# Performance work log

Hardware: AMD Instinct MI355X
Metric: run time of the kernel (lower is better)

The kernel has to match this reference:

```python
import jax, jax.numpy as jnp
import numpy as np

B, U, L, H, M = 4, 16, 128, 768, 256   # docs, utterances/doc, tokens/utt, hidden, mentions/doc
HID = 150                               # Score MLP hidden dim
N_CLUSTERS = 32


def setup_inputs() -> dict:
    key = jax.random.key(0)
    ks = jax.random.split(key, 8)
    hidden = jax.random.normal(ks[0], (B, U, L, H), jnp.float32)

    rng = np.random.default_rng(0)
    span_utt = rng.integers(0, U, (B, M))
    span_start = rng.integers(0, L - 8, (B, M))
    span_end = span_start + rng.integers(1, 9, (B, M))  # span length in [1, 8]

    # coreference labels: label[i, j] = 1 iff j is a true antecedent (j < i, same cluster);
    # if mention i has no antecedent, label[i, i] = 1 (the epsilon / new-entity slot).
    clusters = rng.integers(0, N_CLUSTERS, (B, M))
    same = clusters[:, :, None] == clusters[:, None, :]
    ant = same & np.tril(np.ones((M, M), bool), -1)
    labels = ant.astype(np.float32)
    diag = np.arange(M)
    labels[:, diag, diag] = (~ant.any(-1)).astype(np.float32)

    scale = 0.02
    W1 = jax.random.normal(ks[1], (3 * H, HID), jnp.float32) * scale
    W2 = jax.random.normal(ks[2], (HID, HID), jnp.float32) * scale
    W3 = jax.random.normal(ks[3], (HID, 1), jnp.float32) * scale
    return {
        "hidden": hidden,
        "span_utt": jnp.asarray(span_utt, jnp.int32),
        "span_start": jnp.asarray(span_start, jnp.int32),
        "span_end": jnp.asarray(span_end, jnp.int32),
        "labels": jnp.asarray(labels),
        "W1": W1, "b1": jnp.zeros((HID,), jnp.float32),
        "W2": W2, "b2": jnp.zeros((HID,), jnp.float32),
        "W3": W3, "b3": jnp.zeros((1,), jnp.float32),
    }


def reference(hidden, span_utt, span_start, span_end, labels, W1, b1, W2, b2, W3, b3):
    # ---- span mean-pooling (EntityEncoder, aggr='mean') ----
    pos = jnp.arange(L)
    mask = (pos[None, None, :] >= span_start[..., None]) & (pos[None, None, :] < span_end[..., None])
    w = mask.astype(hidden.dtype) / (span_end - span_start)[..., None].astype(hidden.dtype)  # [B,M,L]
    gathered = jnp.take_along_axis(hidden, span_utt[:, :, None, None], axis=1)  # [B,M,L,H]
    pooled = jnp.einsum('bml,bmlh->bmh', w, gathered)  # [B,M,H]

    # ---- pairwise antecedent scoring (PairScorer / Score MLP, dropout=eval) ----
    ii, jj = np.tril_indices(M, -1)  # static pair indices, P = M(M-1)/2
    # concat(i_g, j_g, i_g*j_g) @ W1  ==  i_g@W1a + j_g@W1b + (i_g*j_g)@W1c
    W1a, W1b, W1c = W1[:H], W1[H:2 * H], W1[2 * H:]
    hi = pooled @ W1a   # [B,M,HID]
    hj = pooled @ W1b   # [B,M,HID]
    prod = pooled[:, ii] * pooled[:, jj]                    # [B,P,H]
    h1 = jax.nn.relu(hi[:, ii] + hj[:, jj] + prod @ W1c + b1)
    h2 = jax.nn.relu(h1 @ W2 + b2)
    s = (h2 @ W3 + b3)[..., 0]  # [B,P]

    # ---- per-mention ragged softmax, padded to [M, M] with -1000 ----
    # row i has logits s_ij for j<i plus epsilon=0 at j=i (diagonal of zeros matrix)
    logits = jnp.zeros((B, M, M), hidden.dtype).at[:, ii, jj].set(s)
    valid = jnp.tril(jnp.ones((M, M), bool))
    probs = jax.nn.softmax(jnp.where(valid, logits, -1e30), axis=-1)
    probs = jnp.where(valid, probs, jnp.asarray(-1000.0, hidden.dtype))

    # ---- compute_loss ----
    eps = 1e-8
    prob_sum = jnp.sum(jnp.clip(probs * labels, eps, 1.0 - eps), axis=-1)  # [B,M]
    loss = -jnp.sum(jnp.log(prob_sum))
    return loss
```

## Files before the change

kernel.cpp:

```cpp
#include <hip/hip_runtime.h>
#include <hip/hip_bf16.h>

#define B_ 4
#define U_ 16
#define L_ 128
#define H_ 768
#define M_ 256
#define HID_ 150

typedef _Float16 half8 __attribute__((ext_vector_type(8)));
typedef _Float16 half4t __attribute__((ext_vector_type(4)));
typedef float floatx4 __attribute__((ext_vector_type(4)));
typedef float floatx16 __attribute__((ext_vector_type(16)));

__global__ __launch_bounds__(256) void prep_kernel(
    const float* __restrict__ W1, const float* __restrict__ W2,
    const float* __restrict__ b2, const float* __restrict__ W3,
    _Float16* __restrict__ W1cs, _Float16* __restrict__ W2s,
    _Float16* __restrict__ W1abs, float2* __restrict__ bw)
{
    int idx = blockIdx.x * 256 + threadIdx.x;
    if (blockIdx.x == 0 && threadIdx.x < 160) {
        int n = threadIdx.x;
        bw[n] = (n < HID_) ? make_float2(b2[n], W3[n]) : make_float2(0.f, 0.f);
    }
    if (idx < 122880) {
        int k = idx / 160, n = idx - k * 160;
        float v = (n < HID_) ? W1[(size_t)(2 * H_ + k) * HID_ + n] : 0.f;
        W1cs[(k >> 4) * 2560 + (n >> 5) * 512 +
             (((n & 31) | (((k >> 3) & 1) << 5)) << 3) + (k & 7)] = (_Float16)v;
        return;
    }
    idx -= 122880;
    if (idx < 25600) {
        int k = idx / 160, n = idx - k * 160;
        float v = (k < HID_ && n < HID_) ? W2[(size_t)k * HID_ + n] : 0.f;
        W2s[(k >> 4) * 2560 + (n >> 5) * 512 +
            (((n & 31) | (((k >> 3) & 1) << 5)) << 3) + (k & 7)] = (_Float16)v;
        return;
    }
    idx -= 25600;
    if (idx < 245760) {
        int k = idx / 320, n = idx - k * 320;
        float v = 0.f;
        if (n < HID_) v = W1[(size_t)k * HID_ + n];
        else if (n >= 160 && n < 160 + HID_) v = W1[(size_t)(H_ + k) * HID_ + (n - 160)];
        W1abs[(k >> 5) * 10240 + (n >> 4) * 512 +
              (((n & 15) | (((k >> 3) & 3) << 4)) << 3) + (k & 7)] = (_Float16)v;
    }
}

__global__ __launch_bounds__(256) void pool_kernel(
    const float* __restrict__ hidden, const int* __restrict__ sutt,
    const int* __restrict__ sstart, const int* __restrict__ send,
    _Float16* __restrict__ pooledh)
{
    const int bm = blockIdx.x * 4 + (threadIdx.x >> 6);
    const int lane = threadIdx.x & 63;
    const int b  = bm >> 8;
    const int u  = sutt[bm];
    const int st = sstart[bm];
    const int en = send[bm];
    const float inv = 1.0f / (float)(en - st);
    const float* src = hidden + ((size_t)(b * U_ + u) * L_) * H_ + lane * 12;
    float4 s[3];
    #pragma unroll
    for (int q = 0; q < 3; ++q) s[q] = make_float4(0.f, 0.f, 0.f, 0.f);
    for (int l = st; l < en; ++l) {
        const float* p = src + (size_t)l * H_;
        #pragma unroll
        for (int q = 0; q < 3; ++q) {
            float4 v = *(const float4*)(p + q * 4);
            s[q].x += v.x; s[q].y += v.y; s[q].z += v.z; s[q].w += v.w;
        }
    }
    _Float16* gp = pooledh + (size_t)bm * H_ + lane * 12;
    #pragma unroll
    for (int q = 0; q < 3; ++q) {
        half4t hv;
        hv[0] = (_Float16)(s[q].x * inv); hv[1] = (_Float16)(s[q].y * inv);
        hv[2] = (_Float16)(s[q].z * inv); hv[3] = (_Float16)(s[q].w * inv);
        *(half4t*)(gp + q * 4) = hv;
    }
}

__global__ __launch_bounds__(256) void hihj_kernel(
    const _Float16* __restrict__ pooledh, const float* __restrict__ b1,
    const _Float16* __restrict__ W1abs,
    float* __restrict__ hiF, float* __restrict__ hjT)
{
    __shared__ __align__(16) _Float16 spool[16 * 776];
    const int blk = blockIdx.x;
    const int tid = threadIdx.x;
    for (int e = tid; e < 16 * 96; e += 256) {
        int r = e / 96, c = e - r * 96;
        *(half8*)&spool[r * 776 + c * 8] =
            *(const half8*)&pooledh[(size_t)(blk * 16 + r) * H_ + c * 8];
    }
    __syncthreads();

    const int w = tid >> 6, lane = tid & 63;
    const int g = lane >> 4, l15 = lane & 15;
    floatx4 acc[5];
    #pragma unroll
    for (int u5 = 0; u5 < 5; ++u5) acc[u5] = (floatx4){0.f, 0.f, 0.f, 0.f};
    const _Float16* aB = &spool[l15 * 776 + g * 8];
    for (int kc = 0; kc < 24; ++kc) {
        half8 av = *(const half8*)(aB + kc * 32);
        #pragma unroll
        for (int u5 = 0; u5 < 5; ++u5) {
            const int u = w * 5 + u5;
            half8 bv = *(const half8*)(W1abs + (size_t)((kc * 20 + u) * 64 + lane) * 8);
            acc[u5] = __builtin_amdgcn_mfma_f32_16x16x32_f16(av, bv, acc[u5], 0, 0, 0);
        }
    }
    const int row0 = blk * 16 + g * 4;
    #pragma unroll
    for (int u5 = 0; u5 < 5; ++u5) {
        const int n = (w * 5 + u5) * 16 + l15;
        if (n < HID_) {
            float b1v = b1[n];
            #pragma unroll
            for (int r = 0; r < 4; ++r)
                hiF[(size_t)(row0 + r) * 160 + n] = acc[u5][r] + b1v;
        } else if (n >= 160 && n < 160 + HID_) {
            *(float4*)&hjT[(size_t)(n - 160) * 1024 + row0] =
                make_float4(acc[u5][0], acc[u5][1], acc[u5][2], acc[u5][3]);
        }
    }
}

__global__ __launch_bounds__(64, 1) void pair_mlp_kernel(
    const _Float16* __restrict__ pooledh,
    const float* __restrict__ hiF, const float* __restrict__ hjT,
    const _Float16* __restrict__ W1cs, const _Float16* __restrict__ W2s,
    const float2* __restrict__ bw, const float* __restrict__ b3,
    float* __restrict__ logits)
{
    __shared__ __align__(16) _Float16 h1L[2 * 32 * 170];

    int q = blockIdx.x;
    const int b = q / 576;
    int r = q - b * 576;
    int jt = 0;
    while (r >= 128 - 16 * jt) { r -= 128 - 16 * jt; ++jt; }
    const int p = 16 * jt + r;
    const int i0 = 2 * p, j0 = jt * 32;
    const int bm = b * M_;
    const int lane = threadIdx.x & 63;
    const int c31 = lane & 31;
    const int hw = lane >> 5;

    const _Float16* pjp  = pooledh + (size_t)(bm + j0 + c31) * H_ + (hw << 3);
    const _Float16* pip0 = pooledh + (size_t)(bm + i0) * H_ + (hw << 3);
    const _Float16* pip1 = pooledh + (size_t)(bm + i0 + 1) * H_ + (hw << 3);

    floatx16 acc1[2][5];
    #pragma unroll
    for (int t = 0; t < 2; ++t)
        #pragma unroll
        for (int t1 = 0; t1 < 5; ++t1)
            #pragma unroll
            for (int e = 0; e < 16; ++e) acc1[t][t1][e] = 0.f;

    half8 Apj0[2], Apj1[2], Ai00[2], Ai01[2], Ai10[2], Ai11[2];
    half8 Wf[2][10];
    #pragma unroll
    for (int c = 0; c < 2; ++c) {
        const int kb = c * 32;
        Apj0[c] = *(const half8*)(pjp + kb);
        Apj1[c] = *(const half8*)(pjp + kb + 16);
        Ai00[c] = *(const half8*)(pip0 + kb);
        Ai01[c] = *(const half8*)(pip0 + kb + 16);
        Ai10[c] = *(const half8*)(pip1 + kb);
        Ai11[c] = *(const half8*)(pip1 + kb + 16);
        const _Float16* wb = W1cs + (size_t)c * 5120 + lane * 8;
        #pragma unroll
        for (int u = 0; u < 10; ++u) Wf[c][u] = *(const half8*)(wb + u * 512);
    }

    for (int kc = 0; kc < 24; ++kc) {
        const int cur = kc & 1;
        half8 npj0, npj1, ni00, ni01, ni10, ni11, nW[10];
        if (kc < 22) {
            const int kb = (kc + 2) * 32;
            npj0 = *(const half8*)(pjp + kb);
            npj1 = *(const half8*)(pjp + kb + 16);
            ni00 = *(const half8*)(pip0 + kb);
            ni01 = *(const half8*)(pip0 + kb + 16);
            ni10 = *(const half8*)(pip1 + kb);
            ni11 = *(const half8*)(pip1 + kb + 16);
            const _Float16* wb = W1cs + (size_t)(kc + 2) * 5120 + lane * 8;
            #pragma unroll
            for (int u = 0; u < 10; ++u) nW[u] = *(const half8*)(wb + u * 512);
        }
        #pragma unroll
        for (int h = 0; h < 2; ++h) {
            half8 pj = h ? Apj1[cur] : Apj0[cur];
            half8 a0 = (h ? Ai01[cur] : Ai00[cur]) * pj;
            half8 a1 = (h ? Ai11[cur] : Ai10[cur]) * pj;
            #pragma unroll
            for (int t1 = 0; t1 < 5; ++t1) {
                half8 wf = Wf[cur][h * 5 + t1];
                acc1[0][t1] = __builtin_amdgcn_mfma_f32_32x32x16_f16(
                    wf, a0, acc1[0][t1], 0, 0, 0);
                acc1[1][t1] = __builtin_amdgcn_mfma_f32_32x32x16_f16(
                    wf, a1, acc1[1][t1], 0, 0, 0);
            }
        }
        if (kc < 22) {
            Apj0[cur] = npj0; Apj1[cur] = npj1;
            Ai00[cur] = ni00; Ai01[cur] = ni01;
            Ai10[cur] = ni10; Ai11[cur] = ni11;
            #pragma unroll
            for (int u = 0; u < 10; ++u) Wf[cur][u] = nW[u];
        }
    }

    #pragma unroll
    for (int t1 = 0; t1 < 5; ++t1) {
        #pragma unroll
        for (int qd = 0; qd < 4; ++qd) {
            const int n1 = t1 * 32 + 8 * qd + 4 * hw;
            float hj0 = hjT[(size_t)(n1 + 0) * 1024 + bm + j0 + c31];
            float hj1 = hjT[(size_t)(n1 + 1) * 1024 + bm + j0 + c31];
            float hj2 = hjT[(size_t)(n1 + 2) * 1024 + bm + j0 + c31];
            float hj3 = hjT[(size_t)(n1 + 3) * 1024 + bm + j0 + c31];
            #pragma unroll
            for (int t = 0; t < 2; ++t) {
                float4 hiv = *(const float4*)&hiF[(size_t)(bm + i0 + t) * 160 + n1];
                half4t hv;
                hv[0] = (_Float16)fmaxf(acc1[t][t1][4 * qd + 0] + hiv.x + hj0, 0.f);
                hv[1] = (_Float16)fmaxf(acc1[t][t1][4 * qd + 1] + hiv.y + hj1, 0.f);
                hv[2] = (_Float16)fmaxf(acc1[t][t1][4 * qd + 2] + hiv.z + hj2, 0.f);
                hv[3] = (_Float16)fmaxf(acc1[t][t1][4 * qd + 3] + hiv.w + hj3, 0.f);
                *(half4t*)&h1L[(t * 32 + c31) * 170 + n1] = hv;
            }
        }
    }
    __syncthreads();

    const float b3v = b3[0];
    #pragma unroll
    for (int t = 0; t < 2; ++t) {
        floatx16 acc2[5];
        #pragma unroll
        for (int t2 = 0; t2 < 5; ++t2)
            #pragma unroll
            for (int e = 0; e < 16; ++e) acc2[t2][e] = 0.f;

        half8 W2b[2][5], h1b[2];
        #pragma unroll
        for (int c = 0; c < 2; ++c) {
            const _Float16* wb = W2s + (size_t)(c * 5) * 512 + lane * 8;
            #pragma unroll
            for (int t2 = 0; t2 < 5; ++t2) W2b[c][t2] = *(const half8*)(wb + t2 * 512);
            h1b[c] = *(const half8*)&h1L[(t * 32 + c31) * 170 + c * 16 + hw * 8];
        }
        for (int kc2 = 0; kc2 < 10; ++kc2) {
            const int cur = kc2 & 1;
            half8 nw[5], nh;
            if (kc2 < 8) {
                const _Float16* wb = W2s + (size_t)((kc2 + 2) * 5) * 512 + lane * 8;
                #pragma unroll
                for (int t2 = 0; t2 < 5; ++t2) nw[t2] = *(const half8*)(wb + t2 * 512);
                nh = *(const half8*)&h1L[(t * 32 + c31) * 170 + (kc2 + 2) * 16 + hw * 8];
            }
            #pragma unroll
            for (int t2 = 0; t2 < 5; ++t2)
                acc2[t2] = __builtin_amdgcn_mfma_f32_32x32x16_f16(
                    W2b[cur][t2], h1b[cur], acc2[t2], 0, 0, 0);
            if (kc2 < 8) {
                #pragma unroll
                for (int t2 = 0; t2 < 5; ++t2) W2b[cur][t2] = nw[t2];
                h1b[cur] = nh;
            }
        }

        float sown = 0.f;
        #pragma unroll
        for (int t2 = 0; t2 < 5; ++t2) {
            #pragma unroll
            for (int qd = 0; qd < 4; ++qd) {
                const int n2 = t2 * 32 + 8 * qd + 4 * hw;
                float4 bw01 = *(const float4*)&bw[n2];
                float4 bw23 = *(const float4*)&bw[n2 + 2];
                sown += fmaxf(acc2[t2][4 * qd + 0] + bw01.x, 0.f) * bw01.y;
                sown += fmaxf(acc2[t2][4 * qd + 1] + bw01.z, 0.f) * bw01.w;
                sown += fmaxf(acc2[t2][4 * qd + 2] + bw23.x, 0.f) * bw23.y;
                sown += fmaxf(acc2[t2][4 * qd + 3] + bw23.z, 0.f) * bw23.w;
            }
        }
        float s = sown + __shfl_xor(sown, 32);
        const int i = i0 + t;
        const int j = j0 + c31;
        if (lane < 32 && j < i)
            logits[(size_t)(bm + i) * M_ + j] = s + b3v;
    }
}

__global__ __launch_bounds__(256) void loss_kernel(
    const float* __restrict__ logits, const float* __restrict__ labels,
    float* __restrict__ out)
{
    const int bm = blockIdx.x;
    const int i  = bm & (M_ - 1);
    const int j  = threadIdx.x;
    __shared__ float red[4];
    __shared__ float bcast;

    float val = (j < i) ? logits[(size_t)bm * M_ + j]
                        : ((j == i) ? 0.0f : -1e30f);

    float m = val;
    #pragma unroll
    for (int off = 32; off >= 1; off >>= 1) m = fmaxf(m, __shfl_down(m, off, 64));
    const int wave = j >> 6, lane = j & 63;
    if (lane == 0) red[wave] = m;
    __syncthreads();
    if (j == 0) bcast = fmaxf(fmaxf(red[0], red[1]), fmaxf(red[2], red[3]));
    __syncthreads();
    const float mm = bcast;

    float e = (j <= i) ? expf(val - mm) : 0.0f;
    float s = e;
    #pragma unroll
    for (int off = 32; off >= 1; off >>= 1) s += __shfl_down(s, off, 64);
    __syncthreads();
    if (lane == 0) red[wave] = s;
    __syncthreads();
    if (j == 0) bcast = red[0] + red[1] + red[2] + red[3];
    __syncthreads();
    const float ssum = bcast;

    float prob = (j <= i) ? (e / ssum) : -1000.0f;
    float lab = labels[(size_t)bm * M_ + j];
    float tv = prob * lab;
    tv = fminf(fmaxf(tv, 1e-8f), 1.0f - 1e-8f);
    float rs = tv;
    #pragma unroll
    for (int off = 32; off >= 1; off >>= 1) rs += __shfl_down(rs, off, 64);
    __syncthreads();
    if (lane == 0) red[wave] = rs;
    __syncthreads();
    if (j == 0) atomicAdd(out, -logf(red[0] + red[1] + red[2] + red[3]));
}

extern "C" void kernel_launch(void* const* d_in, const int* in_sizes, int n_in,
                              void* d_out, int out_size, void* d_ws, size_t ws_size,
                              hipStream_t stream)
{
    const float* hidden = (const float*)d_in[0];
    const int*   sutt   = (const int*)d_in[1];
    const int*   sstart = (const int*)d_in[2];
    const int*   send   = (const int*)d_in[3];
    const float* labels = (const float*)d_in[4];
    const float* W1     = (const float*)d_in[5];
    const float* b1     = (const float*)d_in[6];
    const float* W2     = (const float*)d_in[7];
    const float* b2     = (const float*)d_in[8];
    const float* W3     = (const float*)d_in[9];
    const float* b3     = (const float*)d_in[10];

    float* ws = (float*)d_ws;
    float*    hiF     = ws;
    float*    hjT     = ws + 163840;
    float*    logits  = ws + 327680;
    float2*   bw      = (float2*)(ws + 589824);
    _Float16* pooledh = (_Float16*)(ws + 590144);
    _Float16* W1cs    = (_Float16*)(ws + 983360);
    _Float16* W2s     = (_Float16*)(ws + 1106240);
    _Float16* W1abs   = (_Float16*)(ws + 1119040);
    float* out = (float*)d_out;

    hipMemsetAsync(d_out, 0, sizeof(float), stream);

    prep_kernel<<<dim3(1540), 256, 0, stream>>>(W1, W2, b2, W3,
                                                W1cs, W2s, W1abs, bw);
    pool_kernel<<<dim3(256), 256, 0, stream>>>(hidden, sutt, sstart, send, pooledh);
    hihj_kernel<<<dim3(64), 256, 0, stream>>>(pooledh, b1, W1abs, hiF, hjT);
    pair_mlp_kernel<<<dim3(576 * B_), 64, 0, stream>>>(pooledh, hiF, hjT,
                                                       W1cs, W2s, bw, b3, logits);
    loss_kernel<<<dim3(B_ * M_), 256, 0, stream>>>(logits, labels, out);
}
```

Baseline: 213.7 us.

## Split pair MLP across two waves sharing W1c tiles staged in LDS

The pair MLP block grows from one wave to two, each handling one of the two i-rows. The W1c weight tiles are no longer loaded into every wave's registers. They are now double-buffered in LDS through global_load_lds, so both waves share one copy of each tile. This cuts per-wave register pressure so two blocks can be resident per CU, but it adds a block barrier every k-step and LDS reads of the weight fragments.

```diff
diff --git a/kernel.cpp b/kernel.cpp
--- a/kernel.cpp
+++ b/kernel.cpp
@@ -12,6 +12,13 @@
 typedef _Float16 half4t __attribute__((ext_vector_type(4)));
 typedef float floatx4 __attribute__((ext_vector_type(4)));
 typedef float floatx16 __attribute__((ext_vector_type(16)));
+
+__device__ __forceinline__ void gl_lds16(const _Float16* g, _Float16* l)
+{
+    __builtin_amdgcn_global_load_lds(
+        (const __attribute__((address_space(1))) unsigned int*)g,
+        (__attribute__((address_space(3))) unsigned int*)l, 16, 0, 0);
+}
 
 __global__ __launch_bounds__(256) void prep_kernel(
     const float* __restrict__ W1, const float* __restrict__ W2,
@@ -130,14 +137,14 @@
     }
 }
 
-__global__ __launch_bounds__(64, 1) void pair_mlp_kernel(
+__global__ __launch_bounds__(128, 2) void pair_mlp_kernel(
     const _Float16* __restrict__ pooledh,
     const float* __restrict__ hiF, const float* __restrict__ hjT,
     const _Float16* __restrict__ W1cs, const _Float16* __restrict__ W2s,
     const float2* __restrict__ bw, const float* __restrict__ b3,
     float* __restrict__ logits)
 {
-    __shared__ __align__(16) _Float16 h1L[2 * 32 * 170];
+    __shared__ __align__(16) _Float16 smem[2 * 5440];
 
     int q = blockIdx.x;
     const int b = q / 576;
@@ -147,156 +154,146 @@
     const int p = 16 * jt + r;
     const int i0 = 2 * p, j0 = jt * 32;
     const int bm = b * M_;
+    const int w = threadIdx.x >> 6;
     const int lane = threadIdx.x & 63;
     const int c31 = lane & 31;
     const int hw = lane >> 5;
 
-    const _Float16* pjp  = pooledh + (size_t)(bm + j0 + c31) * H_ + (hw << 3);
-    const _Float16* pip0 = pooledh + (size_t)(bm + i0) * H_ + (hw << 3);
-    const _Float16* pip1 = pooledh + (size_t)(bm + i0 + 1) * H_ + (hw << 3);
-
-    floatx16 acc1[2][5];
-    #pragma unroll
-    for (int t = 0; t < 2; ++t)
-        #pragma unroll
-        for (int t1 = 0; t1 < 5; ++t1)
-            #pragma unroll
-            for (int e = 0; e < 16; ++e) acc1[t][t1][e] = 0.f;
-
-    half8 Apj0[2], Apj1[2], Ai00[2], Ai01[2], Ai10[2], Ai11[2];
-    half8 Wf[2][10];
-    #pragma unroll
-    for (int c = 0; c < 2; ++c) {
-        const int kb = c * 32;
-        Apj0[c] = *(const half8*)(pjp + kb);
-        Apj1[c] = *(const half8*)(pjp + kb + 16);
-        Ai00[c] = *(const half8*)(pip0 + kb);
-        Ai01[c] = *(const half8*)(pip0 + kb + 16);
-        Ai10[c] = *(const half8*)(pip1 + kb);
-        Ai11[c] = *(const half8*)(pip1 + kb + 16);
-        const _Float16* wb = W1cs + (size_t)c * 5120 + lane * 8;
-        #pragma unroll
-        for (int u = 0; u < 10; ++u) Wf[c][u] = *(const half8*)(wb + u * 512);
-    }
+    _Float16* Wb0 = smem;
+    _Float16* Wb1 = smem + 5120;
+    _Float16* h1w = smem + w * 5440;
+
+    const _Float16* pjp = pooledh + (size_t)(bm + j0 + c31) * H_ + (hw << 3);
+    const _Float16* pip = pooledh + (size_t)(bm + i0 + w) * H_ + (hw << 3);
+
+    floatx16 acc1[5];
+    #pragma unroll
+    for (int t1 = 0; t1 < 5; ++t1)
+        #pragma unroll
+        for (int e = 0; e < 16; ++e) acc1[t1][e] = 0.f;
+
+    {
+        const _Float16* gW = W1cs + (size_t)(5 * w) * 512 + lane * 8;
+        #pragma unroll
+        for (int c = 0; c < 5; ++c)
+            gl_lds16(gW + c * 512, Wb0 + (5 * w + c) * 512);
+    }
+    half8 Apj0 = *(const half8*)(pjp);
+    half8 Apj1 = *(const half8*)(pjp + 16);
+    half8 Ai0  = *(const half8*)(pip);
+    half8 Ai1  = *(const half8*)(pip + 16);
+    __syncthreads();
 
     for (int kc = 0; kc < 24; ++kc) {
-        const int cur = kc & 1;
-        half8 npj0, npj1, ni00, ni01, ni10, ni11, nW[10];
-        if (kc < 22) {
-            const int kb = (kc + 2) * 32;
+        const _Float16* Wcur = (kc & 1) ? Wb1 : Wb0;
+        _Float16*       Wnxt = (kc & 1) ? Wb0 : Wb1;
+        half8 npj0, npj1, ni0, ni1;
+        if (kc < 23) {
+            const _Float16* gW = W1cs + (size_t)(kc + 1) * 5120 + (5 * w) * 512 + lane * 8;
+            #pragma unroll
+            for (int c = 0; c < 5; ++c)
+                gl_lds16(gW + c * 512, Wnxt + (5 * w + c) * 512);
+            const int kb = (kc + 1) * 32;
             npj0 = *(const half8*)(pjp + kb);
             npj1 = *(const half8*)(pjp + kb + 16);
-            ni00 = *(const half8*)(pip0 + kb);
-            ni01 = *(const half8*)(pip0 + kb + 16);
-            ni10 = *(const half8*)(pip1 + kb);
-            ni11 = *(const half8*)(pip1 + kb + 16);
-            const _Float16* wb = W1cs + (size_t)(kc + 2) * 5120 + lane * 8;
-            #pragma unroll
-            for (int u = 0; u < 10; ++u) nW[u] = *(const half8*)(wb + u * 512);
-        }
-        #pragma unroll
-        for (int h = 0; h < 2; ++h) {
-            half8 pj = h ? Apj1[cur] : Apj0[cur];
-            half8 a0 = (h ? Ai01[cur] : Ai00[cur]) * pj;
-            half8 a1 = (h ? Ai11[cur] : Ai10[cur]) * pj;
+            ni0  = *(const half8*)(pip + kb);
+            ni1  = *(const half8*)(pip + kb + 16);
+        }
+        {
+            half8 a = Ai0 * Apj0;
             #pragma unroll
             for (int t1 = 0; t1 < 5; ++t1) {
-                half8 wf = Wf[cur][h * 5 + t1];
-                acc1[0][t1] = __builtin_amdgcn_mfma_f32_32x32x16_f16(
-                    wf, a0, acc1[0][t1], 0, 0, 0);
-                acc1[1][t1] = __builtin_amdgcn_mfma_f32_32x32x16_f16(
-                    wf, a1, acc1[1][t1], 0, 0, 0);
+                half8 wf = *(const half8*)&Wcur[t1 * 512 + lane * 8];
+                acc1[t1] = __builtin_amdgcn_mfma_f32_32x32x16_f16(wf, a, acc1[t1], 0, 0, 0);
             }
         }
-        if (kc < 22) {
-            Apj0[cur] = npj0; Apj1[cur] = npj1;
-            Ai00[cur] = ni00; Ai01[cur] = ni01;
-            Ai10[cur] = ni10; Ai11[cur] = ni11;
-            #pragma unroll
-            for (int u = 0; u < 10; ++u) Wf[cur][u] = nW[u];
-        }
-    }
-
+        {
+            half8 a = Ai1 * Apj1;
+            #pragma unroll
+            for (int t1 = 0; t1 < 5; ++t1) {
+                half8 wf = *(const half8*)&Wcur[(5 + t1) * 512 + lane * 8];
+                acc1[t1] = __builtin_amdgcn_mfma_f32_32x32x16_f16(wf, a, acc1[t1], 0, 0, 0);
+            }
+        }
+        if (kc < 23) { Apj0 = npj0; Apj1 = npj1; Ai0 = ni0; Ai1 = ni1; }
+        __syncthreads();
+    }
+
+    const int jcol = bm + j0 + c31;
     #pragma unroll
     for (int t1 = 0; t1 < 5; ++t1) {
         #pragma unroll
         for (int qd = 0; qd < 4; ++qd) {
             const int n1 = t1 * 32 + 8 * qd + 4 * hw;
-            float hj0 = hjT[(size_t)(n1 + 0) * 1024 + bm + j0 + c31];
-            float hj1 = hjT[(size_t)(n1 + 1) * 1024 + bm + j0 + c31];
-            float hj2 = hjT[(size_t)(n1 + 2) * 1024 + bm + j0 + c31];
-            float hj3 = hjT[(size_t)(n1 + 3) * 1024 + bm + j0 + c31];
-            #pragma unroll
-            for (int t = 0; t < 2; ++t) {
-                float4 hiv = *(const float4*)&hiF[(size_t)(bm + i0 + t) * 160 + n1];
-                half4t hv;
-                hv[0] = (_Float16)fmaxf(acc1[t][t1][4 * qd + 0] + hiv.x + hj0, 0.f);
-                hv[1] = (_Float16)fmaxf(acc1[t][t1][4 * qd + 1] + hiv.y + hj1, 0.f);
-                hv[2] = (_Float16)fmaxf(acc1[t][t1][4 * qd + 2] + hiv.z + hj2, 0.f);
-                hv[3] = (_Float16)fmaxf(acc1[t][t1][4 * qd + 3] + hiv.w + hj3, 0.f);
-                *(half4t*)&h1L[(t * 32 + c31) * 170 + n1] = hv;
-            }
+            float hj0 = hjT[(size_t)(n1 + 0) * 1024 + jcol];
+            float hj1 = hjT[(size_t)(n1 + 1) * 1024 + jcol];
+            float hj2 = hjT[(size_t)(n1 + 2) * 1024 + jcol];
+            float hj3 = hjT[(size_t)(n1 + 3) * 1024 + jcol];
+            float4 hiv = *(const float4*)&hiF[(size_t)(bm + i0 + w) * 160 + n1];
+            half4t hv;
+            hv[0] = (_Float16)fmaxf(acc1[t1][4 * qd + 0] + hiv.x + hj0, 0.f);
+            hv[1] = (_Float16)fmaxf(acc1[t1][4 * qd + 1] + hiv.y + hj1, 0.f);
+            hv[2] = (_Float16)fmaxf(acc1[t1][4 * qd + 2] + hiv.z + hj2, 0.f);
+            hv[3] = (_Float16)fmaxf(acc1[t1][4 * qd + 3] + hiv.w + hj3, 0.f);
+            *(half4t*)&h1w[c31 * 170 + n1] = hv;
         }
     }
     __syncthreads();
 
     const float b3v = b3[0];
-    #pragma unroll
-    for (int t = 0; t < 2; ++t) {
-        floatx16 acc2[5];
+    floatx16 acc2[5];
+    #pragma unroll
+    for (int t2 = 0; t2 < 5; ++t2)
+        #pragma unroll
+        for (int e = 0; e < 16; ++e) acc2[t2][e] = 0.f;
+
+    half8 W2b[2][5], h1b[2];
+    #pragma unroll
+    for (int c = 0; c < 2; ++c) {
+        const _Float16* wb = W2s + (size_t)(c * 5) * 512 + lane * 8;
+        #pragma unroll
+        for (int t2 = 0; t2 < 5; ++t2) W2b[c][t2] = *(const half8*)(wb + t2 * 512);
+        h1b[c] = *(const half8*)&h1w[c31 * 170 + c * 16 + hw * 8];
+    }
+    for (int kc2 = 0; kc2 < 10; ++kc2) {
+        const int cur = kc2 & 1;
+        half8 nw[5], nh;
+        if (kc2 < 8) {
+            const _Float16* wb = W2s + (size_t)((kc2 + 2) * 5) * 512 + lane * 8;
+            #pragma unroll
+            for (int t2 = 0; t2 < 5; ++t2) nw[t2] = *(const half8*)(wb + t2 * 512);
+            nh = *(const half8*)&h1w[c31 * 170 + (kc2 + 2) * 16 + hw * 8];
+        }
         #pragma unroll
         for (int t2 = 0; t2 < 5; ++t2)
-            #pragma unroll
-            for (int e = 0; e < 16; ++e) acc2[t2][e] = 0.f;
-
-        half8 W2b[2][5], h1b[2];
-        #pragma unroll
-        for (int c = 0; c < 2; ++c) {
-            const _Float16* wb = W2s + (size_t)(c * 5) * 512 + lane * 8;
-            #pragma unroll
-            for (int t2 = 0; t2 < 5; ++t2) W2b[c][t2] = *(const half8*)(wb + t2 * 512);
-            h1b[c] = *(const half8*)&h1L[(t * 32 + c31) * 170 + c * 16 + hw * 8];
-        }
-        for (int kc2 = 0; kc2 < 10; ++kc2) {
-            const int cur = kc2 & 1;
-            half8 nw[5], nh;
-            if (kc2 < 8) {
-                const _Float16* wb = W2s + (size_t)((kc2 + 2) * 5) * 512 + lane * 8;
-                #pragma unroll
-                for (int t2 = 0; t2 < 5; ++t2) nw[t2] = *(const half8*)(wb + t2 * 512);
-                nh = *(const half8*)&h1L[(t * 32 + c31) * 170 + (kc2 + 2) * 16 + hw * 8];
-            }
-            #pragma unroll
-            for (int t2 = 0; t2 < 5; ++t2)
-                acc2[t2] = __builtin_amdgcn_mfma_f32_32x32x16_f16(
-                    W2b[cur][t2], h1b[cur], acc2[t2], 0, 0, 0);
-            if (kc2 < 8) {
-                #pragma unroll
-                for (int t2 = 0; t2 < 5; ++t2) W2b[cur][t2] = nw[t2];
-                h1b[cur] = nh;
-            }
-        }
-
-        float sown = 0.f;
-        #pragma unroll
-        for (int t2 = 0; t2 < 5; ++t2) {
-            #pragma unroll
-            for (int qd = 0; qd < 4; ++qd) {
-                const int n2 = t2 * 32 + 8 * qd + 4 * hw;
-                float4 bw01 = *(const float4*)&bw[n2];
-                float4 bw23 = *(const float4*)&bw[n2 + 2];
-                sown += fmaxf(acc2[t2][4 * qd + 0] + bw01.x, 0.f) * bw01.y;
-                sown += fmaxf(acc2[t2][4 * qd + 1] + bw01.z, 0.f) * bw01.w;
-                sown += fmaxf(acc2[t2][4 * qd + 2] + bw23.x, 0.f) * bw23.y;
-                sown += fmaxf(acc2[t2][4 * qd + 3] + bw23.z, 0.f) * bw23.w;
-            }
-        }
-        float s = sown + __shfl_xor(sown, 32);
-        const int i = i0 + t;
-        const int j = j0 + c31;
-        if (lane < 32 && j < i)
-            logits[(size_t)(bm + i) * M_ + j] = s + b3v;
-    }
+            acc2[t2] = __builtin_amdgcn_mfma_f32_32x32x16_f16(
+                W2b[cur][t2], h1b[cur], acc2[t2], 0, 0, 0);
+        if (kc2 < 8) {
+            #pragma unroll
+            for (int t2 = 0; t2 < 5; ++t2) W2b[cur][t2] = nw[t2];
+            h1b[cur] = nh;
+        }
+    }
+
+    float sown = 0.f;
+    #pragma unroll
+    for (int t2 = 0; t2 < 5; ++t2) {
+        #pragma unroll
+        for (int qd = 0; qd < 4; ++qd) {
+            const int n2 = t2 * 32 + 8 * qd + 4 * hw;
+            float4 bw01 = *(const float4*)&bw[n2];
+            float4 bw23 = *(const float4*)&bw[n2 + 2];
+            sown += fmaxf(acc2[t2][4 * qd + 0] + bw01.x, 0.f) * bw01.y;
+            sown += fmaxf(acc2[t2][4 * qd + 1] + bw01.z, 0.f) * bw01.w;
+            sown += fmaxf(acc2[t2][4 * qd + 2] + bw23.x, 0.f) * bw23.y;
+            sown += fmaxf(acc2[t2][4 * qd + 3] + bw23.z, 0.f) * bw23.w;
+        }
+    }
+    float s = sown + __shfl_xor(sown, 32);
+    const int i = i0 + w;
+    const int j = j0 + c31;
+    if (lane < 32 && j < i)
+        logits[(size_t)(bm + i) * M_ + j] = s + b3v;
 }
 
 __global__ __launch_bounds__(256) void loss_kernel(
@@ -379,7 +376,7 @@
                                                 W1cs, W2s, W1abs, bw);
     pool_kernel<<<dim3(256), 256, 0, stream>>>(hidden, sutt, sstart, send, pooledh);
     hihj_kernel<<<dim3(64), 256, 0, stream>>>(pooledh, b1, W1abs, hiF, hjT);
-    pair_mlp_kernel<<<dim3(576 * B_), 64, 0, stream>>>(pooledh, hiF, hjT,
-                                                       W1cs, W2s, bw, b3, logits);
+    pair_mlp_kernel<<<dim3(576 * B_), 128, 0, stream>>>(pooledh, hiF, hjT,
+                                                        W1cs, W2s, bw, b3, logits);
     loss_kernel<<<dim3(B_ * M_), 256, 0, stream>>>(logits, labels, out);
 }
```

Result: faster. 202.2 us (-5.4%).
